# Performance work log

Measured on AMD Instinct MI355X. Metric: run time of the kernel, lower is better.

Reference implementation:

```python
import jax, jax.numpy as jnp
import numpy as np
from jax import lax

D_MODEL = 640
D_INNER = 1280
D_STATE = 34
D_CONV = 4
DT_RANK = 40  # ceil(640/16)
DT_MIN, DT_MAX = 1e-3, 1e-1
NUM_LAYERS = 8
BATCH, SEQ = 2, 2048


def setup_inputs() -> dict:
    key = jax.random.key(0)
    ks = jax.random.split(key, 8)
    hidden_states = jax.random.normal(ks[0], (BATCH, SEQ, D_MODEL), dtype=jnp.float32)
    W_in = jax.random.normal(ks[1], (2 * D_INNER, D_MODEL), dtype=jnp.float32) * 0.02
    conv_w = jax.random.normal(ks[2], (D_INNER, D_CONV), dtype=jnp.float32) * 0.2
    conv_b = jnp.zeros((D_INNER,), dtype=jnp.float32)
    W_x = jax.random.normal(ks[3], (DT_RANK + 2 * D_STATE, D_INNER), dtype=jnp.float32) * 0.02
    W_dt = jax.random.normal(ks[4], (D_INNER, DT_RANK), dtype=jnp.float32) * 0.02
    # dt bias init: inverse-softplus of dt sampled log-uniform in [dt_min, dt_max]
    u = jax.random.uniform(ks[5], (D_INNER,), dtype=jnp.float32)
    dt_vals = jnp.exp(u * (np.log(DT_MAX) - np.log(DT_MIN)) + np.log(DT_MIN))
    dt_bias = dt_vals + jnp.log(-jnp.expm1(-dt_vals))
    A_log = jnp.log(jnp.tile(jnp.arange(1, D_STATE + 1, dtype=jnp.float32)[None, :], (D_INNER, 1)))
    D_skip = jnp.ones((D_INNER,), dtype=jnp.float32)
    W_out = jax.random.normal(ks[6], (D_MODEL, D_INNER), dtype=jnp.float32) * (0.02 / np.sqrt(2.0 * NUM_LAYERS))
    return {"hidden_states": hidden_states, "W_in": W_in, "conv_w": conv_w,
            "conv_b": conv_b, "W_x": W_x, "W_dt": W_dt, "dt_bias": dt_bias,
            "A_log": A_log, "D_skip": D_skip, "W_out": W_out}


def _silu(v):
    return v * jax.nn.sigmoid(v)


def _causal_dwconv(x, w, b):
    # x: [B, Di, L], w: [Di, K] depthwise, left-pad K-1 for causality
    out = lax.conv_general_dilated(
        x, w[:, None, :], window_strides=(1,), padding=[(D_CONV - 1, 0)],
        feature_group_count=D_INNER, dimension_numbers=("NCH", "OIH", "NCH"))
    return out + b[None, :, None]


def _selective_scan(u, dt_sp, A, Bm, Cm):
    # u, dt_sp: [B, Di, L]; A: [Di, N]; Bm, Cm: [B, L, N]
    dtl = jnp.moveaxis(dt_sp, 2, 0)  # [L, B, Di]
    ul = jnp.moveaxis(u, 2, 0)       # [L, B, Di]

    def step(h, inp):
        dt_t, u_t, B_t, C_t = inp
        dA = jnp.exp(dt_t[..., None] * A)                   # [B, Di, N]
        h = dA * h + (dt_t * u_t)[..., None] * B_t[:, None, :]
        y = jnp.einsum("bdn,bn->bd", h, C_t)
        return h, y

    h0 = jnp.zeros((u.shape[0], D_INNER, D_STATE), dtype=u.dtype)
    _, ys = lax.scan(step, h0, (dtl, ul, jnp.swapaxes(Bm, 0, 1), jnp.swapaxes(Cm, 0, 1)))
    return jnp.moveaxis(ys, 0, 2)  # [B, Di, L]


def reference(hidden_states, W_in, conv_w, conv_b, W_x, W_dt, dt_bias, A_log, D_skip, W_out):
    # in_proj and split into x / gate z, channels-first
    xz = hidden_states @ W_in.T                    # [B, L, 2*Di]
    x = jnp.swapaxes(xz[..., :D_INNER], 1, 2)      # [B, Di, L]
    z = jnp.swapaxes(xz[..., D_INNER:], 1, 2)      # [B, Di, L]
    # causal depthwise conv + silu
    x = _silu(_causal_dwconv(x, conv_w, conv_b))
    # input-dependent dt, B, C
    x_dbl = jnp.swapaxes(x, 1, 2) @ W_x.T          # [B, L, dt_rank + 2N]
    dt_raw = x_dbl[..., :DT_RANK]
    Bm = x_dbl[..., DT_RANK:DT_RANK + D_STATE]     # [B, L, N]
    Cm = x_dbl[..., DT_RANK + D_STATE:]            # [B, L, N]
    dt = jnp.swapaxes(dt_raw @ W_dt.T, 1, 2)       # [B, Di, L]
    dt_sp = jax.nn.softplus(dt + dt_bias[None, :, None])
    A = -jnp.exp(A_log)                            # [Di, N]
    y = _selective_scan(x, dt_sp, A, Bm, Cm)
    y = y + x * D_skip[None, :, None]
    y = y * _silu(z)
    return jnp.swapaxes(y, 1, 2) @ W_out.T         # [B, L, d_model]
```

## Files before the change

### kernel.cpp

```cpp
#include <hip/hip_runtime.h>
#include <hip/hip_bf16.h>

#define D_MODEL   640
#define D_INNER   1280
#define D_STATE   34
#define D_CONV    4
#define DT_RANK   40
#define BATCH     2
#define SEQ       2048
#define XDBL_W    (DT_RANK + 2 * D_STATE)
#define M_TOTAL   (BATCH * SEQ)
#define NCHUNK    8
#define CHLEN     (SEQ / NCHUNK)
#define RECW      68

typedef __attribute__((ext_vector_type(8))) short short8v;
typedef __attribute__((ext_vector_type(4))) short short4v;
typedef __attribute__((ext_vector_type(4))) float f32x4;

__device__ __forceinline__ void split_bf16(float x, short& hi, short& lo) {
    unsigned u  = __builtin_bit_cast(unsigned, x);
    unsigned uh = u & 0xFFFF0000u;
    hi = (short)(uh >> 16);
    float r = x - __builtin_bit_cast(float, uh);
    unsigned v = __builtin_bit_cast(unsigned, r);
    v += 0x7FFFu + ((v >> 16) & 1u);
    lo = (short)(v >> 16);
}

__device__ __forceinline__ void split4(const float4& v, short4v& h, short4v& l) {
    float xs[4] = {v.x, v.y, v.z, v.w};
    #pragma unroll
    for (int j = 0; j < 4; ++j) { short hh, ll; split_bf16(xs[j], hh, ll); h[j] = hh; l[j] = ll; }
}

template<int MODE>
__global__ __launch_bounds__(256) void gemm_mfma(
    const float* __restrict__ A, const float* __restrict__ B,
    float* __restrict__ C, int M, int N, int K, int lda, int ldb, int ldc)
{
    constexpr int BMt = 128, BKt = 32;
    constexpr int LDT = 40;
    __shared__ short Ahi[BMt * LDT], Alo[BMt * LDT];
    __shared__ short Bhi[BMt * LDT], Blo[BMt * LDT];

    const int tid  = threadIdx.x;
    const long m0  = (long)blockIdx.y * BMt;
    const long n0  = (long)blockIdx.x * BMt;
    const int wid  = tid >> 6, lane = tid & 63;
    const int wr   = (wid >> 1) * 64;
    const int wc   = (wid & 1) * 64;
    const int lrow = lane & 15;
    const int lkb  = lane >> 4;

    const bool do_silu = (MODE == 2) && (m0 >= D_INNER);

    f32x4 acc[4][4] = {};

    for (int k0 = 0; k0 < K; k0 += BKt) {
        __syncthreads();
        #pragma unroll
        for (int q = 0; q < 4; ++q) {
            int flat = tid + q * 256;
            int r  = flat >> 3;
            int f4 = (flat & 7) << 2;
            float4 va = *reinterpret_cast<const float4*>(&A[(m0 + r) * lda + k0 + f4]);
            float4 vb = *reinterpret_cast<const float4*>(&B[(n0 + r) * ldb + k0 + f4]);
            short4v ah, al, bh, bl;
            split4(va, ah, al);
            split4(vb, bh, bl);
            *reinterpret_cast<short4v*>(&Ahi[r * LDT + f4]) = ah;
            *reinterpret_cast<short4v*>(&Alo[r * LDT + f4]) = al;
            *reinterpret_cast<short4v*>(&Bhi[r * LDT + f4]) = bh;
            *reinterpret_cast<short4v*>(&Blo[r * LDT + f4]) = bl;
        }
        __syncthreads();

        short8v a_hi[4], a_lo[4], b_hi[4], b_lo[4];
        #pragma unroll
        for (int i = 0; i < 4; ++i) {
            int ar = (wr + i * 16 + lrow) * LDT + lkb * 8;
            int br = (wc + i * 16 + lrow) * LDT + lkb * 8;
            a_hi[i] = *reinterpret_cast<const short8v*>(&Ahi[ar]);
            a_lo[i] = *reinterpret_cast<const short8v*>(&Alo[ar]);
            b_hi[i] = *reinterpret_cast<const short8v*>(&Bhi[br]);
            b_lo[i] = *reinterpret_cast<const short8v*>(&Blo[br]);
        }
        #pragma unroll
        for (int i = 0; i < 4; ++i)
            #pragma unroll
            for (int j = 0; j < 4; ++j) {
                acc[i][j] = __builtin_amdgcn_mfma_f32_16x16x32_bf16(a_hi[i], b_hi[j], acc[i][j], 0, 0, 0);
                acc[i][j] = __builtin_amdgcn_mfma_f32_16x16x32_bf16(a_hi[i], b_lo[j], acc[i][j], 0, 0, 0);
                acc[i][j] = __builtin_amdgcn_mfma_f32_16x16x32_bf16(a_lo[i], b_hi[j], acc[i][j], 0, 0, 0);
            }
    }

    #pragma unroll
    for (int i = 0; i < 4; ++i) {
        long grow0 = m0 + wr + i * 16 + lkb * 4;
        #pragma unroll
        for (int j = 0; j < 4; ++j) {
            long gcol = n0 + wc + j * 16 + lrow;
            #pragma unroll
            for (int r = 0; r < 4; ++r) {
                float v = acc[i][j][r];
                if (do_silu) v = v * (1.0f / (1.0f + __expf(-v)));
                C[(grow0 + r) * ldc + gcol] = v;
            }
        }
    }
}

#define BM 64
#define BN 64
#define BK 16

template<int LAYA, int MODE>
__global__ __launch_bounds__(256) void gemm_tn(
    const float* __restrict__ A, const float* __restrict__ B,
    float* __restrict__ C, int M, int N, int K, int lda, int ldb, int ldc,
    const float* __restrict__ bias)
{
    __shared__ float As[BK][BM + 4];
    __shared__ float Bs[BK][BN + 4];

    const int tid = threadIdx.x;
    const int m0 = blockIdx.y * BM;
    const int n0 = blockIdx.x * BN;
    const int tx = tid & 15;
    const int ty = tid >> 4;

    float acc[4][4] = {};

    for (int k0 = 0; k0 < K; k0 += BK) {
        #pragma unroll
        for (int i = 0; i < 4; ++i) {
            int idx = tid + i * 256;
            if (LAYA == 0) {
                int r = idx >> 4;
                int c = idx & 15;
                As[c][r] = (m0 + r < M && k0 + c < K)
                         ? A[(long)(m0 + r) * lda + (k0 + c)] : 0.0f;
            } else {
                int c = idx >> 6;
                int r = idx & 63;
                As[c][r] = (m0 + r < M && k0 + c < K)
                         ? A[(long)(k0 + c) * lda + (m0 + r)] : 0.0f;
            }
            int rb = idx >> 4;
            int cb = idx & 15;
            Bs[cb][rb] = (n0 + rb < N && k0 + cb < K)
                       ? B[(long)(n0 + rb) * ldb + (k0 + cb)] : 0.0f;
        }
        __syncthreads();

        #pragma unroll
        for (int k = 0; k < BK; ++k) {
            const float4 a4 = *reinterpret_cast<const float4*>(&As[k][ty * 4]);
            const float4 b4 = *reinterpret_cast<const float4*>(&Bs[k][tx * 4]);
            const float a_[4] = {a4.x, a4.y, a4.z, a4.w};
            const float b_[4] = {b4.x, b4.y, b4.z, b4.w};
            #pragma unroll
            for (int i = 0; i < 4; ++i)
                #pragma unroll
                for (int j = 0; j < 4; ++j)
                    acc[i][j] = fmaf(a_[i], b_[j], acc[i][j]);
        }
        __syncthreads();
    }

    #pragma unroll
    for (int i = 0; i < 4; ++i) {
        int gm = m0 + ty * 4 + i;
        if (gm >= M) continue;
        float bi = (MODE == 2) ? bias[gm] : 0.0f;
        #pragma unroll
        for (int j = 0; j < 4; ++j) {
            int gn = n0 + tx * 4 + j;
            if (gn >= N) continue;
            float v = acc[i][j];
            if (MODE == 2) {
                v += bi;
                v = (v > 15.0f) ? v : log1pf(__expf(v));
            }
            C[(long)gm * ldc + gn] = v;
        }
    }
}

__global__ __launch_bounds__(256) void gemm_splitk(
    const float* __restrict__ A, const float* __restrict__ B,
    float* __restrict__ Cp, int M, int N, int K, int lda, int ldb, int ldc)
{
    __shared__ float As[BK][BM + 4];
    __shared__ float Bs[BK][BN + 4];

    const int tid = threadIdx.x;
    const int m0 = blockIdx.y * BM;
    const int n0 = blockIdx.x * BN;
    const int z  = blockIdx.z;
    const int kseg = K / 4;
    const int kbeg = z * kseg;
    const int tx = tid & 15;
    const int ty = tid >> 4;

    float acc[4][4] = {};

    for (int k0 = kbeg; k0 < kbeg + kseg; k0 += BK) {
        #pragma unroll
        for (int i = 0; i < 4; ++i) {
            int idx = tid + i * 256;
            int c = idx >> 6;
            int r = idx & 63;
            As[c][r] = A[(long)(k0 + c) * lda + (m0 + r)];
            int rb = idx >> 4;
            int cb = idx & 15;
            Bs[cb][rb] = (n0 + rb < N) ? B[(long)(n0 + rb) * ldb + (k0 + cb)] : 0.0f;
        }
        __syncthreads();

        #pragma unroll
        for (int k = 0; k < BK; ++k) {
            const float4 a4 = *reinterpret_cast<const float4*>(&As[k][ty * 4]);
            const float4 b4 = *reinterpret_cast<const float4*>(&Bs[k][tx * 4]);
            const float a_[4] = {a4.x, a4.y, a4.z, a4.w};
            const float b_[4] = {b4.x, b4.y, b4.z, b4.w};
            #pragma unroll
            for (int i = 0; i < 4; ++i)
                #pragma unroll
                for (int j = 0; j < 4; ++j)
                    acc[i][j] = fmaf(a_[i], b_[j], acc[i][j]);
        }
        __syncthreads();
    }

    float* Cz = Cp + (long)z * M * ldc;
    #pragma unroll
    for (int i = 0; i < 4; ++i) {
        int gm = m0 + ty * 4 + i;
        #pragma unroll
        for (int j = 0; j < 4; ++j) {
            int gn = n0 + tx * 4 + j;
            if (gn < N) Cz[(long)gm * ldc + gn] = acc[i][j];
        }
    }
}

__global__ __launch_bounds__(256) void reduce4_kernel(
    const float* __restrict__ part, float* __restrict__ out, int n)
{
    int i4 = (blockIdx.x * 256 + threadIdx.x) * 4;
    if (i4 >= n) return;
    float4 s0 = *reinterpret_cast<const float4*>(&part[i4]);
    float4 s1 = *reinterpret_cast<const float4*>(&part[(long)n + i4]);
    float4 s2 = *reinterpret_cast<const float4*>(&part[(long)2 * n + i4]);
    float4 s3 = *reinterpret_cast<const float4*>(&part[(long)3 * n + i4]);
    float4 r;
    r.x = (s0.x + s1.x) + (s2.x + s3.x);
    r.y = (s0.y + s1.y) + (s2.y + s3.y);
    r.z = (s0.z + s1.z) + (s2.z + s3.z);
    r.w = (s0.w + s1.w) + (s2.w + s3.w);
    *reinterpret_cast<float4*>(&out[i4]) = r;
}

__global__ __launch_bounds__(256) void conv_silu_kernel(
    const float* __restrict__ xT, const float* __restrict__ cw,
    const float* __restrict__ cb, float* __restrict__ uT)
{
    int idx = blockIdx.x * 256 + threadIdx.x;
    if (idx >= D_INNER * M_TOTAL) return;
    int bs = idx & (M_TOTAL - 1);
    int d  = idx >> 12;
    int s  = bs & (SEQ - 1);

    const float* xr = xT + idx;
    float acc = cb[d];
    #pragma unroll
    for (int k = 0; k < D_CONV; ++k) {
        int off = k - (D_CONV - 1);
        if (s + off >= 0)
            acc = fmaf(xr[off], cw[d * D_CONV + k], acc);
    }
    uT[idx] = acc * (1.0f / (1.0f + __expf(-acc)));
}

__global__ __launch_bounds__(256) void transpose_kernel(
    const float* __restrict__ in, float* __restrict__ out)
{
    __shared__ float tile[32][33];
    const int tx = threadIdx.x & 31;
    const int ty = threadIdx.x >> 5;
    const int t0 = blockIdx.x * 32;
    const int d0 = blockIdx.y * 32;

    #pragma unroll
    for (int i = 0; i < 32; i += 8)
        tile[ty + i][tx] = in[(long)(d0 + ty + i) * M_TOTAL + t0 + tx];
    __syncthreads();
    #pragma unroll
    for (int i = 0; i < 32; i += 8)
        out[(long)(t0 + ty + i) * D_INNER + d0 + tx] = tile[tx][ty + i];
}

#define DPP_ADD(X_, CTRL_) {                                                 \
        int t_ = __builtin_amdgcn_update_dpp(                                \
            0, __builtin_bit_cast(int, X_), (CTRL_), 0xf, 0xf, true);        \
        X_ += __builtin_bit_cast(float, t_);                                 \
    }

#define PF 8

__global__ __launch_bounds__(64) void scan_part1(
    const float* __restrict__ xdbl,
    const float* __restrict__ spT,
    const float* __restrict__ A_log,
    const float* __restrict__ uT,
    float* __restrict__ rec)
{
    const int cid  = blockIdx.x;
    const int bd   = cid / (NCHUNK - 1);
    const int c    = cid % (NCHUNK - 1);
    const int lane = threadIdx.x;
    const int b = bd / D_INNER;
    const int d = bd % D_INNER;
    const bool act = lane < D_STATE;

    const float A_n = act ? -__expf(A_log[d * D_STATE + lane]) : 0.0f;

    const long base = (long)d * M_TOTAL + (long)b * SEQ + (long)c * CHLEN;
    const float* sp_p = spT + base;
    const float* u_p  = uT  + base;
    const float* bc_p = xdbl + ((long)b * SEQ + (long)c * CHLEN) * XDBL_W;

    float h = 0.0f, P = 1.0f;

    float aSP[PF], aU[PF], aB[PF];
    float bSP[PF], bU[PF], bB[PF];

#define LOADS1(SP_, U_, B_, T_) {                                            \
        int tt = (T_); tt = (tt < CHLEN) ? tt : (CHLEN - 1);                 \
        SP_ = sp_p[tt];                                                      \
        U_  = u_p [tt];                                                      \
        B_  = act ? bc_p[(long)tt * XDBL_W + DT_RANK + lane] : 0.0f;         \
    }

#define STEP1(SP_, U_, B_) {                                                 \
        float dA = __expf(SP_ * A_n);                                        \
        h = fmaf(dA, h, (SP_ * U_) * B_);                                    \
        P *= dA;                                                             \
    }

    #pragma unroll
    for (int i = 0; i < PF; ++i) LOADS1(aSP[i], aU[i], aB[i], i);

    for (int t0 = 0; t0 < CHLEN; t0 += 2 * PF) {
        #pragma unroll
        for (int i = 0; i < PF; ++i) LOADS1(bSP[i], bU[i], bB[i], t0 + PF + i);
        #pragma unroll
        for (int i = 0; i < PF; ++i) STEP1(aSP[i], aU[i], aB[i]);
        #pragma unroll
        for (int i = 0; i < PF; ++i) LOADS1(aSP[i], aU[i], aB[i], t0 + 2 * PF + i);
        #pragma unroll
        for (int i = 0; i < PF; ++i) STEP1(bSP[i], bU[i], bB[i]);
    }
#undef LOADS1
#undef STEP1

    if (act) {
        rec[(long)cid * RECW + lane]      = h;
        rec[(long)cid * RECW + 34 + lane] = P;
    }
}

__global__ __launch_bounds__(64) void scan_part3(
    const float* __restrict__ gT,
    const float* __restrict__ xdbl,
    const float* __restrict__ spT,
    const float* __restrict__ A_log,
    const float* __restrict__ D_skip,
    const float* __restrict__ rec,
    float* __restrict__ uT)
{
    const int cid  = blockIdx.x;
    const int bd   = cid >> 3;
    const int c    = cid & (NCHUNK - 1);
    const int lane = threadIdx.x;
    const int b = bd / D_INNER;
    const int d = bd % D_INNER;
    const bool act = lane < D_STATE;

    const float A_n = act ? -__expf(A_log[d * D_STATE + lane]) : 0.0f;
    const float Dd  = D_skip[d];

    const long base = (long)d * M_TOTAL + (long)b * SEQ + (long)c * CHLEN;
    const float* sp_p = spT + base;
    const float* g_p  = gT  + base;
    float*       u_p  = uT  + base;
    const float* bc_p = xdbl + ((long)b * SEQ + (long)c * CHLEN) * XDBL_W;

    float h = 0.0f;
    for (int cc = 0; cc < c; ++cc) {
        long rbase = (long)(bd * (NCHUNK - 1) + cc) * RECW;
        float he = act ? rec[rbase + lane]      : 0.0f;
        float Pp = act ? rec[rbase + 34 + lane] : 0.0f;
        h = fmaf(Pp, h, he);
    }

    float aSP[PF], aU[PF], aG[PF], aB[PF], aC[PF];
    float bSP[PF], bU[PF], bG[PF], bB[PF], bC[PF];

#define LOADS(SP_, U_, G_, B_, C_, T_) {                                     \
        int tt = (T_); tt = (tt < CHLEN) ? tt : (CHLEN - 1);                 \
        SP_ = sp_p[tt];                                                      \
        U_  = u_p [tt];                                                      \
        G_  = g_p [tt];                                                      \
        const float* bcq = bc_p + (long)tt * XDBL_W + DT_RANK + lane;        \
        B_ = act ? bcq[0]       : 0.0f;                                      \
        C_ = act ? bcq[D_STATE] : 0.0f;                                      \
    }

#define STEP(SP_, U_, G_, B_, C_, T_) {                                      \
        float dA = __expf(SP_ * A_n);                                        \
        h = fmaf(dA, h, (SP_ * U_) * B_);                                    \
        float pp = h * C_;                                                   \
        DPP_ADD(pp, 0x111);                                  \
        DPP_ADD(pp, 0x112);                                  \
        DPP_ADD(pp, 0x114);                                  \
        DPP_ADD(pp, 0x118);                                  \
        DPP_ADD(pp, 0x142);                                \
        DPP_ADD(pp, 0x143);                                \
        if (lane == 63) {                                                    \
            float y = fmaf(U_, Dd, pp);                                      \
            u_p[T_] = y * G_;                                                \
        }                                                                    \
    }

    #pragma unroll
    for (int i = 0; i < PF; ++i) LOADS(aSP[i], aU[i], aG[i], aB[i], aC[i], i);

    for (int t0 = 0; t0 < CHLEN; t0 += 2 * PF) {
        #pragma unroll
        for (int i = 0; i < PF; ++i)
            LOADS(bSP[i], bU[i], bG[i], bB[i], bC[i], t0 + PF + i);
        #pragma unroll
        for (int i = 0; i < PF; ++i)
            STEP(aSP[i], aU[i], aG[i], aB[i], aC[i], t0 + i);
        #pragma unroll
        for (int i = 0; i < PF; ++i)
            LOADS(aSP[i], aU[i], aG[i], aB[i], aC[i], t0 + 2 * PF + i);
        #pragma unroll
        for (int i = 0; i < PF; ++i)
            STEP(bSP[i], bU[i], bG[i], bB[i], bC[i], t0 + PF + i);
    }
#undef LOADS
#undef STEP
}

extern "C" void kernel_launch(void* const* d_in, const int* in_sizes, int n_in,
                              void* d_out, int out_size, void* d_ws, size_t ws_size,
                              hipStream_t stream)
{
    const float* hs      = (const float*)d_in[0];
    const float* W_in    = (const float*)d_in[1];
    const float* conv_w  = (const float*)d_in[2];
    const float* conv_b  = (const float*)d_in[3];
    const float* W_x     = (const float*)d_in[4];
    const float* W_dt    = (const float*)d_in[5];
    const float* dt_bias = (const float*)d_in[6];
    const float* A_log   = (const float*)d_in[7];
    const float* D_skip  = (const float*)d_in[8];
    const float* W_out   = (const float*)d_in[9];
    float* out = (float*)d_out;

    float* ws   = (float*)d_ws;
    float* xT   = ws;
    float* gT   = xT   + (size_t)D_INNER * M_TOTAL;
    float* uT   = gT   + (size_t)D_INNER * M_TOTAL;
    float* xdbl = uT   + (size_t)D_INNER * M_TOTAL;
    float* spT  = xdbl + (size_t)M_TOTAL * XDBL_W;
    float* rec  = spT  + (size_t)D_INNER * M_TOTAL;
    float* part = xT;
    float* yN   = xT;

    dim3 blk(256);

    gemm_mfma<2><<<dim3(M_TOTAL / 128, (2 * D_INNER) / 128), blk, 0, stream>>>(
        W_in, hs, xT, 2 * D_INNER, M_TOTAL, D_MODEL, D_MODEL, D_MODEL, M_TOTAL);

    conv_silu_kernel<<<(D_INNER * M_TOTAL + 255) / 256, blk, 0, stream>>>(
        xT, conv_w, conv_b, uT);

    gemm_splitk<<<dim3((XDBL_W + BN - 1) / BN, M_TOTAL / BM, 4), blk, 0, stream>>>(
        uT, W_x, part, M_TOTAL, XDBL_W, D_INNER, M_TOTAL, D_INNER, XDBL_W);

    reduce4_kernel<<<(M_TOTAL * XDBL_W / 4 + 255) / 256, blk, 0, stream>>>(
        part, xdbl, M_TOTAL * XDBL_W);

    gemm_tn<0, 2><<<dim3(M_TOTAL / BN, D_INNER / BM), blk, 0, stream>>>(
        W_dt, xdbl, spT, D_INNER, M_TOTAL, DT_RANK, DT_RANK, XDBL_W, M_TOTAL,
        dt_bias);

    scan_part1<<<BATCH * D_INNER * (NCHUNK - 1), 64, 0, stream>>>(
        xdbl, spT, A_log, uT, rec);

    scan_part3<<<BATCH * D_INNER * NCHUNK, 64, 0, stream>>>(
        gT, xdbl, spT, A_log, D_skip, rec, uT);

    transpose_kernel<<<dim3(M_TOTAL / 32, D_INNER / 32), blk, 0, stream>>>(uT, yN);

    gemm_mfma<0><<<dim3(D_MODEL / 128, M_TOTAL / 128), blk, 0, stream>>>(
        yN, W_out, out, M_TOTAL, D_MODEL, D_INNER, D_INNER, D_INNER, D_MODEL);
}
```

Baseline: 657.8 us.

## Store x_dbl channel-major and vectorize scan loads with float4

The x_proj output is now written transposed (channel-major over tokens), so the B and C coefficients for each state lane are contiguous in time. The split-K GEMM, the dt GEMM's B-operand loader and both scan kernels are changed to match. The scan kernels now load sp/u/g/B/C as float4 per four timesteps instead of scalar strided loads, and lane 63 writes outputs as float4. This is meant to cut uncoalesced strided reads of B/C inside the serial scan, at the cost of a smaller prefetch depth and a changed GEMM access pattern.

Measured after the change: 629.9 us. -4.2%, faster.

```diff
diff --git a/kernel.cpp b/kernel.cpp
--- a/kernel.cpp
+++ b/kernel.cpp
@@ -12,6 +12,7 @@
 #define M_TOTAL   (BATCH * SEQ)
 #define NCHUNK    8
 #define CHLEN     (SEQ / NCHUNK)
+#define NQ        (CHLEN / 4)
 #define RECW      68
 
 typedef __attribute__((ext_vector_type(8))) short short8v;
@@ -116,7 +117,7 @@
 #define BN 64
 #define BK 16
 
-template<int LAYA, int MODE>
+template<int LAYA, int LAYB, int MODE>
 __global__ __launch_bounds__(256) void gemm_tn(
     const float* __restrict__ A, const float* __restrict__ B,
     float* __restrict__ C, int M, int N, int K, int lda, int ldb, int ldc,
@@ -148,10 +149,17 @@
                 As[c][r] = (m0 + r < M && k0 + c < K)
                          ? A[(long)(k0 + c) * lda + (m0 + r)] : 0.0f;
             }
-            int rb = idx >> 4;
-            int cb = idx & 15;
-            Bs[cb][rb] = (n0 + rb < N && k0 + cb < K)
-                       ? B[(long)(n0 + rb) * ldb + (k0 + cb)] : 0.0f;
+            if (LAYB == 0) {
+                int rb = idx >> 4;
+                int cb = idx & 15;
+                Bs[cb][rb] = (n0 + rb < N && k0 + cb < K)
+                           ? B[(long)(n0 + rb) * ldb + (k0 + cb)] : 0.0f;
+            } else {
+                int cb = idx >> 6;
+                int rb = idx & 63;
+                Bs[cb][rb] = (n0 + rb < N && k0 + cb < K)
+                           ? B[(long)(k0 + cb) * ldb + (n0 + rb)] : 0.0f;
+            }
         }
         __syncthreads();
 
@@ -189,7 +197,7 @@
     }
 }
 
-__global__ __launch_bounds__(256) void gemm_splitk(
+__global__ __launch_bounds__(256) void gemm_splitk_T(
     const float* __restrict__ A, const float* __restrict__ B,
     float* __restrict__ Cp, int M, int N, int K, int lda, int ldb, int ldc)
 {
@@ -211,12 +219,12 @@
         #pragma unroll
         for (int i = 0; i < 4; ++i) {
             int idx = tid + i * 256;
-            int c = idx >> 6;
-            int r = idx & 63;
-            As[c][r] = A[(long)(k0 + c) * lda + (m0 + r)];
-            int rb = idx >> 4;
-            int cb = idx & 15;
-            Bs[cb][rb] = (n0 + rb < N) ? B[(long)(n0 + rb) * ldb + (k0 + cb)] : 0.0f;
+            int r = idx >> 4;
+            int c = idx & 15;
+            As[c][r] = (m0 + r < M) ? A[(long)(m0 + r) * lda + (k0 + c)] : 0.0f;
+            int cb = idx >> 6;
+            int rb = idx & 63;
+            Bs[cb][rb] = B[(long)(k0 + cb) * ldb + (n0 + rb)];
         }
         __syncthreads();
 
@@ -239,10 +247,11 @@
     #pragma unroll
     for (int i = 0; i < 4; ++i) {
         int gm = m0 + ty * 4 + i;
+        if (gm >= M) continue;
         #pragma unroll
         for (int j = 0; j < 4; ++j) {
             int gn = n0 + tx * 4 + j;
-            if (gn < N) Cz[(long)gm * ldc + gn] = acc[i][j];
+            Cz[(long)gm * ldc + gn] = acc[i][j];
         }
     }
 }
@@ -309,10 +318,8 @@
         X_ += __builtin_bit_cast(float, t_);                                 \
     }
 
-#define PF 8
-
 __global__ __launch_bounds__(64) void scan_part1(
-    const float* __restrict__ xdbl,
+    const float* __restrict__ xdblT,
     const float* __restrict__ spT,
     const float* __restrict__ A_log,
     const float* __restrict__ uT,
@@ -328,44 +335,44 @@
 
     const float A_n = act ? -__expf(A_log[d * D_STATE + lane]) : 0.0f;
 
-    const long base = (long)d * M_TOTAL + (long)b * SEQ + (long)c * CHLEN;
-    const float* sp_p = spT + base;
-    const float* u_p  = uT  + base;
-    const float* bc_p = xdbl + ((long)b * SEQ + (long)c * CHLEN) * XDBL_W;
+    const long tbase = (long)b * SEQ + (long)c * CHLEN;
+    const float* sp_p = spT + (long)d * M_TOTAL + tbase;
+    const float* u_p  = uT  + (long)d * M_TOTAL + tbase;
+    const float* Bp   = xdblT + (long)(act ? DT_RANK + lane : 0) * M_TOTAL + tbase;
 
     float h = 0.0f, P = 1.0f;
 
-    float aSP[PF], aU[PF], aB[PF];
-    float bSP[PF], bU[PF], bB[PF];
-
-#define LOADS1(SP_, U_, B_, T_) {                                            \
-        int tt = (T_); tt = (tt < CHLEN) ? tt : (CHLEN - 1);                 \
-        SP_ = sp_p[tt];                                                      \
-        U_  = u_p [tt];                                                      \
-        B_  = act ? bc_p[(long)tt * XDBL_W + DT_RANK + lane] : 0.0f;         \
-    }
-
-#define STEP1(SP_, U_, B_) {                                                 \
-        float dA = __expf(SP_ * A_n);                                        \
-        h = fmaf(dA, h, (SP_ * U_) * B_);                                    \
+    float4 aSP, aU, aB, bSP, bU, bB;
+
+#define LOADQ1(SP_, U_, B_, Q_) {                                            \
+        int qq = (Q_); qq = (qq < NQ) ? qq : (NQ - 1); int tt = qq * 4;      \
+        SP_ = *reinterpret_cast<const float4*>(&sp_p[tt]);                   \
+        U_  = *reinterpret_cast<const float4*>(&u_p[tt]);                    \
+        B_  = *reinterpret_cast<const float4*>(&Bp[tt]);                     \
+        if (!act) B_ = make_float4(0.f, 0.f, 0.f, 0.f);                      \
+    }
+
+#define ST1(SPX, UX, BX) {                                                   \
+        float dA = __expf((SPX) * A_n);                                      \
+        h = fmaf(dA, h, ((SPX) * (UX)) * (BX));                              \
         P *= dA;                                                             \
     }
 
-    #pragma unroll
-    for (int i = 0; i < PF; ++i) LOADS1(aSP[i], aU[i], aB[i], i);
-
-    for (int t0 = 0; t0 < CHLEN; t0 += 2 * PF) {
-        #pragma unroll
-        for (int i = 0; i < PF; ++i) LOADS1(bSP[i], bU[i], bB[i], t0 + PF + i);
-        #pragma unroll
-        for (int i = 0; i < PF; ++i) STEP1(aSP[i], aU[i], aB[i]);
-        #pragma unroll
-        for (int i = 0; i < PF; ++i) LOADS1(aSP[i], aU[i], aB[i], t0 + 2 * PF + i);
-        #pragma unroll
-        for (int i = 0; i < PF; ++i) STEP1(bSP[i], bU[i], bB[i]);
-    }
-#undef LOADS1
-#undef STEP1
+#define STEPQ1(SP_, U_, B_) {                                                \
+        ST1(SP_.x, U_.x, B_.x); ST1(SP_.y, U_.y, B_.y);                      \
+        ST1(SP_.z, U_.z, B_.z); ST1(SP_.w, U_.w, B_.w);                      \
+    }
+
+    LOADQ1(aSP, aU, aB, 0);
+    for (int q = 0; q < NQ; q += 2) {
+        LOADQ1(bSP, bU, bB, q + 1);
+        STEPQ1(aSP, aU, aB);
+        LOADQ1(aSP, aU, aB, q + 2);
+        STEPQ1(bSP, bU, bB);
+    }
+#undef LOADQ1
+#undef ST1
+#undef STEPQ1
 
     if (act) {
         rec[(long)cid * RECW + lane]      = h;
@@ -375,7 +382,7 @@
 
 __global__ __launch_bounds__(64) void scan_part3(
     const float* __restrict__ gT,
-    const float* __restrict__ xdbl,
+    const float* __restrict__ xdblT,
     const float* __restrict__ spT,
     const float* __restrict__ A_log,
     const float* __restrict__ D_skip,
@@ -393,11 +400,12 @@
     const float A_n = act ? -__expf(A_log[d * D_STATE + lane]) : 0.0f;
     const float Dd  = D_skip[d];
 
-    const long base = (long)d * M_TOTAL + (long)b * SEQ + (long)c * CHLEN;
-    const float* sp_p = spT + base;
-    const float* g_p  = gT  + base;
-    float*       u_p  = uT  + base;
-    const float* bc_p = xdbl + ((long)b * SEQ + (long)c * CHLEN) * XDBL_W;
+    const long tbase = (long)b * SEQ + (long)c * CHLEN;
+    const float* sp_p = spT + (long)d * M_TOTAL + tbase;
+    const float* g_p  = gT  + (long)d * M_TOTAL + tbase;
+    float*       u_p  = uT  + (long)d * M_TOTAL + tbase;
+    const float* Bp   = xdblT + (long)(act ? DT_RANK + lane : 0) * M_TOTAL + tbase;
+    const float* Cp   = xdblT + (long)(act ? DT_RANK + D_STATE + lane : 0) * M_TOTAL + tbase;
 
     float h = 0.0f;
     for (int cc = 0; cc < c; ++cc) {
@@ -407,54 +415,52 @@
         h = fmaf(Pp, h, he);
     }
 
-    float aSP[PF], aU[PF], aG[PF], aB[PF], aC[PF];
-    float bSP[PF], bU[PF], bG[PF], bB[PF], bC[PF];
-
-#define LOADS(SP_, U_, G_, B_, C_, T_) {                                     \
-        int tt = (T_); tt = (tt < CHLEN) ? tt : (CHLEN - 1);                 \
-        SP_ = sp_p[tt];                                                      \
-        U_  = u_p [tt];                                                      \
-        G_  = g_p [tt];                                                      \
-        const float* bcq = bc_p + (long)tt * XDBL_W + DT_RANK + lane;        \
-        B_ = act ? bcq[0]       : 0.0f;                                      \
-        C_ = act ? bcq[D_STATE] : 0.0f;                                      \
-    }
-
-#define STEP(SP_, U_, G_, B_, C_, T_) {                                      \
-        float dA = __expf(SP_ * A_n);                                        \
-        h = fmaf(dA, h, (SP_ * U_) * B_);                                    \
-        float pp = h * C_;                                                   \
+    float4 aSP, aU, aG, aB, aC, bSP, bU, bG, bB, bC;
+
+#define LOADQ(SP_, U_, G_, B_, C_, Q_) {                                     \
+        int qq = (Q_); qq = (qq < NQ) ? qq : (NQ - 1); int tt = qq * 4;      \
+        SP_ = *reinterpret_cast<const float4*>(&sp_p[tt]);                   \
+        U_  = *reinterpret_cast<const float4*>(&u_p[tt]);                    \
+        G_  = *reinterpret_cast<const float4*>(&g_p[tt]);                    \
+        B_  = *reinterpret_cast<const float4*>(&Bp[tt]);                     \
+        C_  = *reinterpret_cast<const float4*>(&Cp[tt]);                     \
+        if (!act) { B_ = make_float4(0.f,0.f,0.f,0.f);                       \
+                    C_ = make_float4(0.f,0.f,0.f,0.f); }                     \
+    }
+
+#define ST(SPX, UX, GX, BX, CX, YX) {                                        \
+        float dA = __expf((SPX) * A_n);                                      \
+        h = fmaf(dA, h, ((SPX) * (UX)) * (BX));                              \
+        float pp = h * (CX);                                                 \
         DPP_ADD(pp, 0x111);                                  \
         DPP_ADD(pp, 0x112);                                  \
         DPP_ADD(pp, 0x114);                                  \
         DPP_ADD(pp, 0x118);                                  \
         DPP_ADD(pp, 0x142);                                \
         DPP_ADD(pp, 0x143);                                \
-        if (lane == 63) {                                                    \
-            float y = fmaf(U_, Dd, pp);                                      \
-            u_p[T_] = y * G_;                                                \
-        }                                                                    \
-    }
-
-    #pragma unroll
-    for (int i = 0; i < PF; ++i) LOADS(aSP[i], aU[i], aG[i], aB[i], aC[i], i);
-
-    for (int t0 = 0; t0 < CHLEN; t0 += 2 * PF) {
-        #pragma unroll
-        for (int i = 0; i < PF; ++i)
-            LOADS(bSP[i], bU[i], bG[i], bB[i], bC[i], t0 + PF + i);
-        #pragma unroll
-        for (int i = 0; i < PF; ++i)
-            STEP(aSP[i], aU[i], aG[i], aB[i], aC[i], t0 + i);
-        #pragma unroll
-        for (int i = 0; i < PF; ++i)
-            LOADS(aSP[i], aU[i], aG[i], aB[i], aC[i], t0 + 2 * PF + i);
-        #pragma unroll
-        for (int i = 0; i < PF; ++i)
-            STEP(bSP[i], bU[i], bG[i], bB[i], bC[i], t0 + PF + i);
-    }
-#undef LOADS
-#undef STEP
+        YX = fmaf((UX), Dd, pp) * (GX);                                      \
+    }
+
+#define STEPQ(SP_, U_, G_, B_, C_, Q_) {                                     \
+        float4 yq;                                                           \
+        ST(SP_.x, U_.x, G_.x, B_.x, C_.x, yq.x);                             \
+        ST(SP_.y, U_.y, G_.y, B_.y, C_.y, yq.y);                             \
+        ST(SP_.z, U_.z, G_.z, B_.z, C_.z, yq.z);                             \
+        ST(SP_.w, U_.w, G_.w, B_.w, C_.w, yq.w);                             \
+        if (lane == 63)                                                      \
+            *reinterpret_cast<float4*>(&u_p[(Q_) * 4]) = yq;                 \
+    }
+
+    LOADQ(aSP, aU, aG, aB, aC, 0);
+    for (int q = 0; q < NQ; q += 2) {
+        LOADQ(bSP, bU, bG, bB, bC, q + 1);
+        STEPQ(aSP, aU, aG, aB, aC, q);
+        LOADQ(aSP, aU, aG, aB, aC, q + 2);
+        STEPQ(bSP, bU, bG, bB, bC, q + 1);
+    }
+#undef LOADQ
+#undef ST
+#undef STEPQ
 }
 
 extern "C" void kernel_launch(void* const* d_in, const int* in_sizes, int n_in,
@@ -473,15 +479,15 @@
     const float* W_out   = (const float*)d_in[9];
     float* out = (float*)d_out;
 
-    float* ws   = (float*)d_ws;
-    float* xT   = ws;
-    float* gT   = xT   + (size_t)D_INNER * M_TOTAL;
-    float* uT   = gT   + (size_t)D_INNER * M_TOTAL;
-    float* xdbl = uT   + (size_t)D_INNER * M_TOTAL;
-    float* spT  = xdbl + (size_t)M_TOTAL * XDBL_W;
-    float* rec  = spT  + (size_t)D_INNER * M_TOTAL;
-    float* part = xT;
-    float* yN   = xT;
+    float* ws    = (float*)d_ws;
+    float* xT    = ws;
+    float* gT    = xT    + (size_t)D_INNER * M_TOTAL;
+    float* uT    = gT    + (size_t)D_INNER * M_TOTAL;
+    float* xdblT = uT    + (size_t)D_INNER * M_TOTAL;
+    float* spT   = xdblT + (size_t)XDBL_W * M_TOTAL;
+    float* rec   = spT   + (size_t)D_INNER * M_TOTAL;
+    float* part  = xT;
+    float* yN    = xT;
 
     dim3 blk(256);
 
@@ -491,21 +497,21 @@
     conv_silu_kernel<<<(D_INNER * M_TOTAL + 255) / 256, blk, 0, stream>>>(
         xT, conv_w, conv_b, uT);
 
-    gemm_splitk<<<dim3((XDBL_W + BN - 1) / BN, M_TOTAL / BM, 4), blk, 0, stream>>>(
-        uT, W_x, part, M_TOTAL, XDBL_W, D_INNER, M_TOTAL, D_INNER, XDBL_W);
-
-    reduce4_kernel<<<(M_TOTAL * XDBL_W / 4 + 255) / 256, blk, 0, stream>>>(
-        part, xdbl, M_TOTAL * XDBL_W);
-
-    gemm_tn<0, 2><<<dim3(M_TOTAL / BN, D_INNER / BM), blk, 0, stream>>>(
-        W_dt, xdbl, spT, D_INNER, M_TOTAL, DT_RANK, DT_RANK, XDBL_W, M_TOTAL,
+    gemm_splitk_T<<<dim3(M_TOTAL / BN, (XDBL_W + BM - 1) / BM, 4), blk, 0, stream>>>(
+        W_x, uT, part, XDBL_W, M_TOTAL, D_INNER, D_INNER, M_TOTAL, M_TOTAL);
+
+    reduce4_kernel<<<(XDBL_W * M_TOTAL / 4 + 255) / 256, blk, 0, stream>>>(
+        part, xdblT, XDBL_W * M_TOTAL);
+
+    gemm_tn<0, 1, 2><<<dim3(M_TOTAL / BN, D_INNER / BM), blk, 0, stream>>>(
+        W_dt, xdblT, spT, D_INNER, M_TOTAL, DT_RANK, DT_RANK, M_TOTAL, M_TOTAL,
         dt_bias);
 
     scan_part1<<<BATCH * D_INNER * (NCHUNK - 1), 64, 0, stream>>>(
-        xdbl, spT, A_log, uT, rec);
+        xdblT, spT, A_log, uT, rec);
 
     scan_part3<<<BATCH * D_INNER * NCHUNK, 64, 0, stream>>>(
-        gT, xdbl, spT, A_log, D_skip, rec, uT);
+        gT, xdblT, spT, A_log, D_skip, rec, uT);
 
     transpose_kernel<<<dim3(M_TOTAL / 32, D_INNER / 32), blk, 0, stream>>>(uT, yN);
 
```
